# Kernel optimization log

Measured on AMD Instinct MI355X. Metric: run time of the kernel, lower is better.

The kernel has to match this reference:

```python
import jax, jax.numpy as jnp
import numpy as np
import math

S, B, H, NH = 2048, 2, 2048, 16
HN = H // NH  # head dim = 128

def setup_inputs() -> dict:
    key = jax.random.key(0)
    ks = jax.random.split(key, 5)
    hidden_states = jax.random.normal(ks[0], (S, B, H), dtype=jnp.float32)
    # causal mask: True means masked (filled with -10000), broadcast over heads
    attention_mask = jnp.triu(jnp.ones((S, S), dtype=bool), k=1)[None, None].repeat(B, axis=0)
    w_qkv = jax.random.normal(ks[1], (3 * H, H), dtype=jnp.float32) * (1.0 / math.sqrt(H))
    b_qkv = jax.random.normal(ks[2], (3 * H,), dtype=jnp.float32) * 0.02
    w_dense = jax.random.normal(ks[3], (H, H), dtype=jnp.float32) * (1.0 / math.sqrt(H))
    b_dense = jax.random.normal(ks[4], (H,), dtype=jnp.float32) * 0.02
    return {"hidden_states": hidden_states, "attention_mask": attention_mask,
            "w_qkv": w_qkv, "b_qkv": b_qkv, "w_dense": w_dense, "b_dense": b_dense}

def reference(hidden_states, attention_mask, w_qkv, b_qkv, w_dense, b_dense):
    s, b, h = hidden_states.shape
    nh, hn = NH, h // NH
    # QKV projection (ColumnParallelLinear, world_size=1)
    qkv = hidden_states @ w_qkv.T + b_qkv                # [s, b, 3h]
    qkv = qkv.reshape(s, b, nh, 3 * hn)
    q, k, v = jnp.split(qkv, 3, axis=-1)                 # each [s, b, nh, hn]
    q = q.transpose(1, 2, 0, 3)                          # [b, nh, s, hn]
    k = k.transpose(1, 2, 0, 3)
    v = v.transpose(1, 2, 0, 3)
    # norm_factor = sqrt(hn)*coeff, softmax rescales by coeff -> net 1/sqrt(hn)
    scores = jnp.einsum('bnqh,bnkh->bnqk', q, k) / jnp.float32(math.sqrt(hn))
    scores = jnp.where(attention_mask, jnp.float32(-10000.0), scores)
    probs = jax.nn.softmax(scores, axis=-1)              # [b, nh, s, s]
    ctx = jnp.einsum('bnqk,bnkh->bnqh', probs, v)        # [b, nh, s, hn]
    ctx = ctx.transpose(2, 0, 1, 3).reshape(s, b, h)     # [s, b, h]
    # RowParallelLinear with skip_bias_add=True: bias returned separately
    output = ctx @ w_dense.T
    return output, b_dense
```

## Files before the change

kernel.cpp:

```cpp
#include <hip/hip_runtime.h>

typedef unsigned short u16;
typedef unsigned int   u32;
typedef __attribute__((ext_vector_type(8))) short bf16x8;
typedef __attribute__((ext_vector_type(4))) float f32x4;

#define S_LEN 2048
#define B_SZ  2
#define H_DIM 2048
#define NH_   16
#define HN_   128
#define M_TOK 4096
#define NQKV  6144
#define NT_   (S_LEN / 64)

#define LGKM_BARRIER asm volatile("s_waitcnt lgkmcnt(0)\n\ts_barrier" ::: "memory")
#define SCHED_FENCE  asm volatile("" ::: "memory")

__device__ __forceinline__ u16 f2bf(float f) {
    u32 x = __float_as_uint(f);
    return (u16)((x + 0x7fffu + ((x >> 16) & 1u)) >> 16);
}

__device__ __forceinline__ void async16(const void* g, void* l) {
    __builtin_amdgcn_global_load_lds((const __attribute__((address_space(1))) void*)g,
                                     (__attribute__((address_space(3))) void*)l,
                                     16, 0, 0);
}

__global__ __launch_bounds__(256) void cvt3(
    const float* __restrict__ a, u16* __restrict__ oa, int na,
    const float* __restrict__ b, u16* __restrict__ ob, int nb,
    const float* __restrict__ c, u16* __restrict__ oc, int nc)
{
    int g = blockIdx.x * 256 + threadIdx.x;
    const float* in; u16* out; int idx;
    if (g < na)           { in = a; out = oa; idx = g; }
    else if (g < na + nb) { in = b; out = ob; idx = g - na; }
    else if (g < na + nb + nc) { in = c; out = oc; idx = g - na - nb; }
    else return;
    int i = idx * 4;
    float4 v = *(const float4*)&in[i];
    ushort4 o;
    o.x = f2bf(v.x); o.y = f2bf(v.y); o.z = f2bf(v.z); o.w = f2bf(v.w);
    *(ushort4*)&out[i] = o;
}

template<int EPI>
__global__ __launch_bounds__(256) void gemm_rs(
    const u16* __restrict__ A, const u16* __restrict__ W,
    const float* __restrict__ bias, float* __restrict__ Cout,
    u16* __restrict__ Qb, u16* __restrict__ Kb, u16* __restrict__ Vt,
    int M, int N, int K)
{
    __shared__ __align__(16) u16 Af[2][8 * 64 * 8];
    __shared__ __align__(16) u16 Bf[2][8 * 64 * 8];
    const int t = threadIdx.x, l = t & 63, w = t >> 6;
    const int quad = l >> 4, ln = l & 15;
    const int wm = w >> 1, wn = w & 1;
    const int m0 = blockIdx.y * 128, n0 = blockIdx.x * 128;

    const int c0 = t, c1 = t + 256;
    const u16* pa0 = &A[(size_t)(m0 + (c0 >> 6) * 16 + (c0 & 15)) * K + ((c0 >> 4) & 3) * 8];
    const u16* pa1 = &A[(size_t)(m0 + (c1 >> 6) * 16 + (c1 & 15)) * K + ((c1 >> 4) & 3) * 8];
    const u16* pb0 = &W[(size_t)(n0 + (c0 >> 6) * 16 + (c0 & 15)) * K + ((c0 >> 4) & 3) * 8];
    const u16* pb1 = &W[(size_t)(n0 + (c1 >> 6) * 16 + (c1 & 15)) * K + ((c1 >> 4) & 3) * 8];

    f32x4 acc[4][4];
#pragma unroll
    for (int i = 0; i < 4; ++i)
#pragma unroll
        for (int j = 0; j < 4; ++j)
#pragma unroll
            for (int r = 0; r < 4; ++r) acc[i][j][r] = 0.f;

    bf16x8 xa0, xa1, xb0, xb1;
    bf16x8 ya0, ya1, yb0, yb1;

#define LD_TILE(k0, a0, a1, b0, b1)                 \
    do {                                            \
        a0 = *(const bf16x8*)(pa0 + (k0));          \
        a1 = *(const bf16x8*)(pa1 + (k0));          \
        b0 = *(const bf16x8*)(pb0 + (k0));          \
        b1 = *(const bf16x8*)(pb1 + (k0));          \
        SCHED_FENCE;                                \
    } while (0)

#define ST_TILE(buf, a0, a1, b0, b1)                \
    do {                                            \
        *(bf16x8*)&Af[buf][t * 8]        = a0;      \
        *(bf16x8*)&Af[buf][t * 8 + 2048] = a1;      \
        *(bf16x8*)&Bf[buf][t * 8]        = b0;      \
        *(bf16x8*)&Bf[buf][t * 8 + 2048] = b1;      \
    } while (0)

#define COMPUTE(buf)                                                          \
    do {                                                                      \
        bf16x8 af[4], bfr[4];                                                 \
        _Pragma("unroll")                                                     \
        for (int x = 0; x < 4; ++x) {                                         \
            af[x]  = *(const bf16x8*)&Af[buf][((wm * 4 + x) * 64 + l) * 8];   \
            bfr[x] = *(const bf16x8*)&Bf[buf][((wn * 4 + x) * 64 + l) * 8];   \
        }                                                                     \
        _Pragma("unroll")                                                     \
        for (int mt = 0; mt < 4; ++mt)                                        \
            _Pragma("unroll")                                                 \
            for (int nt = 0; nt < 4; ++nt)                                    \
                acc[mt][nt] = __builtin_amdgcn_mfma_f32_16x16x32_bf16(        \
                    af[mt], bfr[nt], acc[mt][nt], 0, 0, 0);                   \
    } while (0)

    const int NIT = K / 32;

    LD_TILE(0, xa0, xa1, xb0, xb1);
    ST_TILE(0, xa0, xa1, xb0, xb1);
    LD_TILE(32, ya0, ya1, yb0, yb1);
    LGKM_BARRIER;

#pragma unroll 1
    for (int kk = 0; kk < NIT; kk += 2) {
        if (kk + 2 < NIT) LD_TILE((kk + 2) * 32, xa0, xa1, xb0, xb1);
        COMPUTE(0);
        ST_TILE(1, ya0, ya1, yb0, yb1);
        LGKM_BARRIER;
        if (kk + 3 < NIT) LD_TILE((kk + 3) * 32, ya0, ya1, yb0, yb1);
        COMPUTE(1);
        if (kk + 2 < NIT) ST_TILE(0, xa0, xa1, xb0, xb1);
        LGKM_BARRIER;
    }
#undef LD_TILE
#undef ST_TILE
#undef COMPUTE

    if constexpr (EPI == 0) {
#pragma unroll
        for (int mt = 0; mt < 4; ++mt)
#pragma unroll
            for (int nt = 0; nt < 4; ++nt) {
                int col = n0 + (wn * 4 + nt) * 16 + ln;
#pragma unroll
                for (int r = 0; r < 4; ++r) {
                    int row = m0 + wm * 64 + mt * 16 + quad * 4 + r;
                    Cout[(size_t)row * N + col] = acc[mt][nt][r];
                }
            }
    } else {
        const float kQS = 0.08838834764831845f * 1.44269504088896340f;
#pragma unroll
        for (int nt = 0; nt < 4; ++nt) {
            int col  = n0 + (wn * 4 + nt) * 16 + ln;
            int head = col / 384;
            int g    = col - head * 384;
            int sec  = g >> 7;
            int d    = g & 127;
            float bv = bias[col];
#pragma unroll
            for (int mt = 0; mt < 4; ++mt)
#pragma unroll
                for (int r = 0; r < 4; ++r) {
                    int tok = m0 + wm * 64 + mt * 16 + quad * 4 + r;
                    int s = tok >> 1, bb = tok & 1;
                    float v = acc[mt][nt][r] + bv;
                    if (sec == 0)
                        Qb[((size_t)(bb * NH_ + head) * S_LEN + s) * HN_ + d] = f2bf(v * kQS);
                    else if (sec == 1)
                        Kb[((size_t)(bb * NH_ + head) * S_LEN + s) * HN_ + d] = f2bf(v);
                    else
                        Vt[((size_t)(bb * NH_ + head) * HN_ + d) * S_LEN + s] = f2bf(v);
                }
        }
    }
}

__global__ __launch_bounds__(256) void attn_mfma(
    const u16* __restrict__ Qb, const u16* __restrict__ Kb,
    const u16* __restrict__ Vt, u16* __restrict__ Ctx)
{
    __shared__ __align__(16) u16 Ks[2][16 * 64 * 8];
    __shared__ __align__(16) u16 Vs[2][16 * 64 * 8];
    __shared__ __align__(16) u16 Psm[4][16][72];

    const int t = threadIdx.x, l = t & 63, w = t >> 6;
    const int quad = l >> 4, ln = l & 15;
    const int j = blockIdx.x;
    const int n = blockIdx.y, b = blockIdx.z;
    const u16* Qh = Qb + (size_t)(b * NH_ + n) * S_LEN * HN_;
    const u16* Kh = Kb + (size_t)(b * NH_ + n) * S_LEN * HN_;
    const u16* Vh = Vt + (size_t)(b * NH_ + n) * HN_ * S_LEN;

#pragma unroll 1
    for (int phase = 0; phase < 2; ++phase) {
        const int qt = phase ? j : (NT_ - 1 - j);
        const int q0 = qt * 64;

#pragma unroll
        for (int i = 0; i < 4; ++i)
            async16(&Qh[(size_t)(q0 + i * 16 + ln) * HN_ + w * 32 + quad * 8],
                    &Ks[1][((i * 4 + w) * 64 + l) * 8]);
#pragma unroll
        for (int i = 0; i < 4; ++i) {
            async16(&Kh[(size_t)(i * 16 + ln) * HN_ + w * 32 + quad * 8],
                    &Ks[0][((i * 4 + w) * 64 + l) * 8]);
            int dv = i * 4 + w, dt = dv >> 1, ks = dv & 1;
            async16(&Vh[(size_t)(dt * 16 + ln) * S_LEN + ks * 32 + quad * 8],
                    &Vs[0][(dv * 64 + l) * 8]);
        }
        __syncthreads();

        bf16x8 qf[4];
#pragma unroll
        for (int ks = 0; ks < 4; ++ks)
            qf[ks] = *(const bf16x8*)&Ks[1][((w * 4 + ks) * 64 + l) * 8];
        __syncthreads();

        float m_i[4], l_i[4];
        f32x4 acco[8];
#pragma unroll
        for (int r = 0; r < 4; ++r) { m_i[r] = -1e30f; l_i[r] = 0.f; }
#pragma unroll
        for (int dt = 0; dt < 8; ++dt)
#pragma unroll
            for (int r = 0; r < 4; ++r) acco[dt][r] = 0.f;

#pragma unroll 1
        for (int kt = 0; kt <= qt; ++kt) {
            const int cur = kt & 1;

            if (kt < qt) {
                const int nxt = cur ^ 1;
#pragma unroll
                for (int i = 0; i < 4; ++i) {
                    async16(&Kh[(size_t)((kt + 1) * 64 + i * 16 + ln) * HN_ + w * 32 + quad * 8],
                            &Ks[nxt][((i * 4 + w) * 64 + l) * 8]);
                    int dv = i * 4 + w, dt = dv >> 1, ks = dv & 1;
                    async16(&Vh[(size_t)(dt * 16 + ln) * S_LEN + (kt + 1) * 64 + ks * 32 + quad * 8],
                            &Vs[nxt][(dv * 64 + l) * 8]);
                }
            }

            f32x4 sc[4];
#pragma unroll
            for (int nt = 0; nt < 4; ++nt)
#pragma unroll
                for (int r = 0; r < 4; ++r) sc[nt][r] = 0.f;
#pragma unroll
            for (int nt = 0; nt < 4; ++nt)
#pragma unroll
                for (int ks = 0; ks < 4; ++ks) {
                    bf16x8 kf = *(const bf16x8*)&Ks[cur][((nt * 4 + ks) * 64 + l) * 8];
                    sc[nt] = __builtin_amdgcn_mfma_f32_16x16x32_bf16(qf[ks], kf, sc[nt], 0, 0, 0);
                }

            if (kt == qt) {
#pragma unroll
                for (int nt = 0; nt < 4; ++nt)
#pragma unroll
                    for (int r = 0; r < 4; ++r)
                        if (nt * 16 + ln > w * 16 + quad * 4 + r) sc[nt][r] = -1e30f;
            }

            float corr[4];
#pragma unroll
            for (int r = 0; r < 4; ++r) {
                float mx = fmaxf(fmaxf(sc[0][r], sc[1][r]), fmaxf(sc[2][r], sc[3][r]));
                mx = fmaxf(mx, __shfl_xor(mx, 1));
                mx = fmaxf(mx, __shfl_xor(mx, 2));
                mx = fmaxf(mx, __shfl_xor(mx, 4));
                mx = fmaxf(mx, __shfl_xor(mx, 8));
                float mnew = fmaxf(m_i[r], mx);
                corr[r] = exp2f(m_i[r] - mnew);
                m_i[r] = mnew;
            }
#pragma unroll
            for (int r = 0; r < 4; ++r) {
                float ps = 0.f;
#pragma unroll
                for (int nt = 0; nt < 4; ++nt) {
                    float p = exp2f(sc[nt][r] - m_i[r]);
                    ps += p;
                    Psm[w][quad * 4 + r][nt * 16 + ln] = f2bf(p);
                }
                l_i[r] = l_i[r] * corr[r] + ps;
            }

#pragma unroll
            for (int dt = 0; dt < 8; ++dt)
#pragma unroll
                for (int r = 0; r < 4; ++r) acco[dt][r] *= corr[r];

            bf16x8 pf[2];
#pragma unroll
            for (int ks = 0; ks < 2; ++ks)
                pf[ks] = *(const bf16x8*)&Psm[w][ln][ks * 32 + quad * 8];
#pragma unroll
            for (int dt = 0; dt < 8; ++dt)
#pragma unroll
                for (int ks = 0; ks < 2; ++ks) {
                    bf16x8 vf = *(const bf16x8*)&Vs[cur][((dt * 2 + ks) * 64 + l) * 8];
                    acco[dt] = __builtin_amdgcn_mfma_f32_16x16x32_bf16(pf[ks], vf, acco[dt], 0, 0, 0);
                }
            __syncthreads();
        }

#pragma unroll
        for (int r = 0; r < 4; ++r) {
            float s = l_i[r];
            s += __shfl_xor(s, 1);
            s += __shfl_xor(s, 2);
            s += __shfl_xor(s, 4);
            s += __shfl_xor(s, 8);
            l_i[r] = 1.f / s;
        }
#pragma unroll
        for (int dt = 0; dt < 8; ++dt)
#pragma unroll
            for (int r = 0; r < 4; ++r) {
                int srow = q0 + w * 16 + quad * 4 + r;
                Ctx[((size_t)(srow * B_SZ + b)) * H_DIM + n * HN_ + dt * 16 + ln] =
                    f2bf(acco[dt][r] * l_i[r]);
            }
    }
}

__global__ void copy_bias(const float* __restrict__ b_dense, float* __restrict__ out)
{
    int t = blockIdx.x * 256 + threadIdx.x;
    if (t < H_DIM) out[(size_t)M_TOK * H_DIM + t] = b_dense[t];
}

extern "C" void kernel_launch(void* const* d_in, const int* in_sizes, int n_in,
                              void* d_out, int out_size, void* d_ws, size_t ws_size,
                              hipStream_t stream)
{
    const float* hs      = (const float*)d_in[0];
    const float* w_qkv   = (const float*)d_in[2];
    const float* b_qkv   = (const float*)d_in[3];
    const float* w_dense = (const float*)d_in[4];
    const float* b_dense = (const float*)d_in[5];
    float* out = (float*)d_out;

    u16* hs_bf = (u16*)d_ws;
    u16* wq_bf = hs_bf + (size_t)M_TOK * H_DIM;
    u16* wd_bf = wq_bf + (size_t)NQKV * H_DIM;
    u16* Qb    = wd_bf + (size_t)H_DIM * H_DIM;
    u16* Kb    = Qb    + (size_t)M_TOK * H_DIM;
    u16* Vt    = Kb    + (size_t)M_TOK * H_DIM;
    u16* Ctx   = Vt    + (size_t)M_TOK * H_DIM;

    const int g1 = (M_TOK * H_DIM) / 4;
    const int g2 = (NQKV * H_DIM) / 4;
    const int g3 = (H_DIM * H_DIM) / 4;
    cvt3<<<(g1 + g2 + g3 + 255) / 256, 256, 0, stream>>>(
        hs, hs_bf, g1, w_qkv, wq_bf, g2, w_dense, wd_bf, g3);

    gemm_rs<1><<<dim3(NQKV / 128, M_TOK / 128), 256, 0, stream>>>(
        hs_bf, wq_bf, b_qkv, nullptr, Qb, Kb, Vt, M_TOK, NQKV, H_DIM);

    attn_mfma<<<dim3(NT_ / 2, NH_, B_SZ), 256, 0, stream>>>(Qb, Kb, Vt, Ctx);

    gemm_rs<0><<<dim3(H_DIM / 128, M_TOK / 128), 256, 0, stream>>>(
        Ctx, wd_bf, nullptr, out, nullptr, nullptr, nullptr, M_TOK, H_DIM, H_DIM);

    copy_bias<<<(H_DIM + 255) / 256, 256, 0, stream>>>(b_dense, out);
}
```

Measured before the change: 502.6 us.

## Replace GEMM with 256x256 tiled 8-wave kernel using async LDS loads and swizzle

Both projection GEMMs now use a new kernel with 256x256 output tiles, 512 threads, and 64-wide K steps. Tiles go straight from global memory into XOR-swizzled shared memory through async loads, interleaved with MFMA quarter-blocks under raised wave priority. Workgroups are remapped so that neighbouring blocks land across XCDs. The aim is more data reuse per tile, fewer LDS bank conflicts, and latency hidden behind compute. The cost is heavier register and shared-memory use, many barriers, and sizes hardcoded at compile time.

New measurement: 450.4 us. 1.12x faster.

```diff
diff --git a/kernel.cpp b/kernel.cpp
--- a/kernel.cpp
+++ b/kernel.cpp
@@ -14,8 +14,8 @@
 #define NQKV  6144
 #define NT_   (S_LEN / 64)
 
-#define LGKM_BARRIER asm volatile("s_waitcnt lgkmcnt(0)\n\ts_barrier" ::: "memory")
-#define SCHED_FENCE  asm volatile("" ::: "memory")
+#define BAR      asm volatile("s_barrier" ::: "memory")
+#define WAITV(n) asm volatile("s_waitcnt vmcnt(" #n ")" ::: "memory")
 
 __device__ __forceinline__ u16 f2bf(float f) {
     u32 x = __float_as_uint(f);
@@ -46,128 +46,185 @@
     *(ushort4*)&out[i] = o;
 }
 
-template<int EPI>
-__global__ __launch_bounds__(256) void gemm_rs(
+template<int EPI, int MM, int NN>
+__global__ __launch_bounds__(512, 2) void gemm8(
     const u16* __restrict__ A, const u16* __restrict__ W,
     const float* __restrict__ bias, float* __restrict__ Cout,
-    u16* __restrict__ Qb, u16* __restrict__ Kb, u16* __restrict__ Vt,
-    int M, int N, int K)
+    u16* __restrict__ Qb, u16* __restrict__ Kb, u16* __restrict__ Vt)
 {
-    __shared__ __align__(16) u16 Af[2][8 * 64 * 8];
-    __shared__ __align__(16) u16 Bf[2][8 * 64 * 8];
+    constexpr int K   = 2048;
+    constexpr int NKT = K / 64;
+    constexpr int NBN = NN / 256;
+    constexpr int NWG = (MM / 256) * NBN;
+
+    __shared__ __align__(16) u16 sA[2][256 * 64];
+    __shared__ __align__(16) u16 sB[2][256 * 64];
+
     const int t = threadIdx.x, l = t & 63, w = t >> 6;
     const int quad = l >> 4, ln = l & 15;
-    const int wm = w >> 1, wn = w & 1;
-    const int m0 = blockIdx.y * 128, n0 = blockIdx.x * 128;
-
-    const int c0 = t, c1 = t + 256;
-    const u16* pa0 = &A[(size_t)(m0 + (c0 >> 6) * 16 + (c0 & 15)) * K + ((c0 >> 4) & 3) * 8];
-    const u16* pa1 = &A[(size_t)(m0 + (c1 >> 6) * 16 + (c1 & 15)) * K + ((c1 >> 4) & 3) * 8];
-    const u16* pb0 = &W[(size_t)(n0 + (c0 >> 6) * 16 + (c0 & 15)) * K + ((c0 >> 4) & 3) * 8];
-    const u16* pb1 = &W[(size_t)(n0 + (c1 >> 6) * 16 + (c1 & 15)) * K + ((c1 >> 4) & 3) * 8];
-
-    f32x4 acc[4][4];
-#pragma unroll
-    for (int i = 0; i < 4; ++i)
-#pragma unroll
-        for (int j = 0; j < 4; ++j)
-#pragma unroll
-            for (int r = 0; r < 4; ++r) acc[i][j][r] = 0.f;
-
-    bf16x8 xa0, xa1, xb0, xb1;
-    bf16x8 ya0, ya1, yb0, yb1;
-
-#define LD_TILE(k0, a0, a1, b0, b1)                 \
-    do {                                            \
-        a0 = *(const bf16x8*)(pa0 + (k0));          \
-        a1 = *(const bf16x8*)(pa1 + (k0));          \
-        b0 = *(const bf16x8*)(pb0 + (k0));          \
-        b1 = *(const bf16x8*)(pb1 + (k0));          \
-        SCHED_FENCE;                                \
+    const int qw_r = w >> 2, qw_c = w & 3;
+
+    int wg = blockIdx.x;
+    wg = (wg & 7) * (NWG / 8) + (wg >> 3);
+    const int m0 = (wg / NBN) * 256, n0 = (wg % NBN) * 256;
+
+    const int srow = t >> 3;
+    const int skc  = (t & 7) ^ (srow & 7);
+    const u16* pA = A + (size_t)(m0 + srow) * K + skc * 8;
+    const u16* pB = W + (size_t)(n0 + srow) * K + skc * 8;
+
+#define STAGE_A(db, h, kt)                                                        \
+    do {                                                                          \
+        async16(pA + (size_t)(h) * 128 * K + (size_t)(kt) * 64,                   \
+                &sA[db][(h) * 8192 + t * 8]);                                     \
+        async16(pA + (size_t)(h) * 128 * K + (size_t)64 * K + (size_t)(kt) * 64,  \
+                &sA[db][(h) * 8192 + t * 8 + 4096]);                              \
     } while (0)
-
-#define ST_TILE(buf, a0, a1, b0, b1)                \
-    do {                                            \
-        *(bf16x8*)&Af[buf][t * 8]        = a0;      \
-        *(bf16x8*)&Af[buf][t * 8 + 2048] = a1;      \
-        *(bf16x8*)&Bf[buf][t * 8]        = b0;      \
-        *(bf16x8*)&Bf[buf][t * 8 + 2048] = b1;      \
+#define STAGE_B(db, h, kt)                                                        \
+    do {                                                                          \
+        async16(pB + (size_t)(h) * 128 * K + (size_t)(kt) * 64,                   \
+                &sB[db][(h) * 8192 + t * 8]);                                     \
+        async16(pB + (size_t)(h) * 128 * K + (size_t)64 * K + (size_t)(kt) * 64,  \
+                &sB[db][(h) * 8192 + t * 8 + 4096]);                              \
     } while (0)
 
-#define COMPUTE(buf)                                                          \
-    do {                                                                      \
-        bf16x8 af[4], bfr[4];                                                 \
-        _Pragma("unroll")                                                     \
-        for (int x = 0; x < 4; ++x) {                                         \
-            af[x]  = *(const bf16x8*)&Af[buf][((wm * 4 + x) * 64 + l) * 8];   \
-            bfr[x] = *(const bf16x8*)&Bf[buf][((wn * 4 + x) * 64 + l) * 8];   \
-        }                                                                     \
-        _Pragma("unroll")                                                     \
-        for (int mt = 0; mt < 4; ++mt)                                        \
-            _Pragma("unroll")                                                 \
-            for (int nt = 0; nt < 4; ++nt)                                    \
-                acc[mt][nt] = __builtin_amdgcn_mfma_f32_16x16x32_bf16(        \
-                    af[mt], bfr[nt], acc[mt][nt], 0, 0, 0);                   \
+    const int aBase = (qw_r * 64 + ln) * 64;
+    const int bBase = (qw_c * 32 + ln) * 64;
+    int swz[2];
+#pragma unroll
+    for (int ks = 0; ks < 2; ++ks)
+        swz[ks] = ((ks * 4 + quad) ^ (ln & 7)) << 3;
+
+    bf16x8 af[4][2];
+    bf16x8 bf[2][2];
+
+#define RD_A(db, mq)                                                              \
+    do {                                                                          \
+        _Pragma("unroll") for (int mf = 0; mf < 4; ++mf)                          \
+        _Pragma("unroll") for (int ks = 0; ks < 2; ++ks)                          \
+            af[mf][ks] = *(const bf16x8*)&sA[db][aBase + (mq) * 8192 + mf * 1024  \
+                                                + swz[ks]];                       \
     } while (0)
-
-    const int NIT = K / 32;
-
-    LD_TILE(0, xa0, xa1, xb0, xb1);
-    ST_TILE(0, xa0, xa1, xb0, xb1);
-    LD_TILE(32, ya0, ya1, yb0, yb1);
-    LGKM_BARRIER;
+#define RD_B(db, nq)                                                              \
+    do {                                                                          \
+        _Pragma("unroll") for (int nf = 0; nf < 2; ++nf)                          \
+        _Pragma("unroll") for (int ks = 0; ks < 2; ++ks)                          \
+            bf[nf][ks] = *(const bf16x8*)&sB[db][bBase + (nq) * 8192 + nf * 1024  \
+                                                + swz[ks]];                       \
+    } while (0)
+
+    f32x4 acc[4][4][2];
+#pragma unroll
+    for (int q = 0; q < 4; ++q)
+#pragma unroll
+        for (int mf = 0; mf < 4; ++mf)
+#pragma unroll
+            for (int nf = 0; nf < 2; ++nf)
+#pragma unroll
+                for (int r = 0; r < 4; ++r) acc[q][mf][nf][r] = 0.f;
+
+#define MM16(q)                                                                   \
+    do {                                                                          \
+        __builtin_amdgcn_s_setprio(1);                                            \
+        _Pragma("unroll") for (int mf = 0; mf < 4; ++mf)                          \
+        _Pragma("unroll") for (int nf = 0; nf < 2; ++nf)                          \
+        _Pragma("unroll") for (int ks = 0; ks < 2; ++ks)                          \
+            acc[q][mf][nf] = __builtin_amdgcn_mfma_f32_16x16x32_bf16(             \
+                af[mf][ks], bf[nf][ks], acc[q][mf][nf], 0, 0, 0);                 \
+        __builtin_amdgcn_s_setprio(0);                                            \
+    } while (0)
+
+    STAGE_A(0, 0, 0); STAGE_B(0, 0, 0); STAGE_A(0, 1, 0); STAGE_B(0, 1, 0);
+    STAGE_A(1, 0, 1); STAGE_B(1, 0, 1);
+    WAITV(4);
+    BAR;
 
 #pragma unroll 1
-    for (int kk = 0; kk < NIT; kk += 2) {
-        if (kk + 2 < NIT) LD_TILE((kk + 2) * 32, xa0, xa1, xb0, xb1);
-        COMPUTE(0);
-        ST_TILE(1, ya0, ya1, yb0, yb1);
-        LGKM_BARRIER;
-        if (kk + 3 < NIT) LD_TILE((kk + 3) * 32, ya0, ya1, yb0, yb1);
-        COMPUTE(1);
-        if (kk + 2 < NIT) ST_TILE(0, xa0, xa1, xb0, xb1);
-        LGKM_BARRIER;
+    for (int i = 0; i < NKT / 2; ++i) {
+        const int tt  = 2 * i;
+        const int tp1 = tt + 1;
+        const int tp2 = (tt + 2) & (NKT - 1);
+        const int tp3 = (tt + 3) & (NKT - 1);
+
+        RD_A(0, 0); RD_B(0, 0);
+        STAGE_A(1, 1, tp1);
+        BAR; MM16(0); BAR;
+        RD_B(0, 1);
+        STAGE_B(1, 1, tp1);
+        BAR; MM16(1); BAR;
+        RD_A(0, 1); RD_B(0, 0);
+        STAGE_A(0, 0, tp2);
+        BAR; MM16(2); BAR;
+        RD_B(0, 1);
+        STAGE_B(0, 0, tp2);
+        BAR; MM16(3);
+        WAITV(4);
+        BAR;
+        RD_A(1, 0); RD_B(1, 0);
+        STAGE_A(0, 1, tp2);
+        BAR; MM16(0); BAR;
+        RD_B(1, 1);
+        STAGE_B(0, 1, tp2);
+        BAR; MM16(1); BAR;
+        RD_A(1, 1); RD_B(1, 0);
+        STAGE_A(1, 0, tp3);
+        BAR; MM16(2); BAR;
+        RD_B(1, 1);
+        STAGE_B(1, 0, tp3);
+        BAR; MM16(3);
+        WAITV(4);
+        BAR;
     }
-#undef LD_TILE
-#undef ST_TILE
-#undef COMPUTE
+#undef STAGE_A
+#undef STAGE_B
+#undef RD_A
+#undef RD_B
+#undef MM16
 
     if constexpr (EPI == 0) {
 #pragma unroll
-        for (int mt = 0; mt < 4; ++mt)
-#pragma unroll
-            for (int nt = 0; nt < 4; ++nt) {
-                int col = n0 + (wn * 4 + nt) * 16 + ln;
-#pragma unroll
-                for (int r = 0; r < 4; ++r) {
-                    int row = m0 + wm * 64 + mt * 16 + quad * 4 + r;
-                    Cout[(size_t)row * N + col] = acc[mt][nt][r];
+        for (int q = 0; q < 4; ++q) {
+            const int mq = q >> 1, nq = q & 1;
+#pragma unroll
+            for (int mf = 0; mf < 4; ++mf)
+#pragma unroll
+                for (int nf = 0; nf < 2; ++nf) {
+                    int col = n0 + nq * 128 + qw_c * 32 + nf * 16 + ln;
+#pragma unroll
+                    for (int r = 0; r < 4; ++r) {
+                        int row = m0 + mq * 128 + qw_r * 64 + mf * 16 + quad * 4 + r;
+                        Cout[(size_t)row * NN + col] = acc[q][mf][nf][r];
+                    }
                 }
-            }
+        }
     } else {
         const float kQS = 0.08838834764831845f * 1.44269504088896340f;
 #pragma unroll
-        for (int nt = 0; nt < 4; ++nt) {
-            int col  = n0 + (wn * 4 + nt) * 16 + ln;
-            int head = col / 384;
-            int g    = col - head * 384;
-            int sec  = g >> 7;
-            int d    = g & 127;
-            float bv = bias[col];
-#pragma unroll
-            for (int mt = 0; mt < 4; ++mt)
-#pragma unroll
-                for (int r = 0; r < 4; ++r) {
-                    int tok = m0 + wm * 64 + mt * 16 + quad * 4 + r;
-                    int s = tok >> 1, bb = tok & 1;
-                    float v = acc[mt][nt][r] + bv;
-                    if (sec == 0)
-                        Qb[((size_t)(bb * NH_ + head) * S_LEN + s) * HN_ + d] = f2bf(v * kQS);
-                    else if (sec == 1)
-                        Kb[((size_t)(bb * NH_ + head) * S_LEN + s) * HN_ + d] = f2bf(v);
-                    else
-                        Vt[((size_t)(bb * NH_ + head) * HN_ + d) * S_LEN + s] = f2bf(v);
-                }
+        for (int q = 0; q < 4; ++q) {
+            const int mq = q >> 1, nq = q & 1;
+#pragma unroll
+            for (int nf = 0; nf < 2; ++nf) {
+                int col  = n0 + nq * 128 + qw_c * 32 + nf * 16 + ln;
+                int head = col / 384;
+                int g    = col - head * 384;
+                int sec  = g >> 7;
+                int d    = g & 127;
+                float bv = bias[col];
+#pragma unroll
+                for (int mf = 0; mf < 4; ++mf)
+#pragma unroll
+                    for (int r = 0; r < 4; ++r) {
+                        int tok = m0 + mq * 128 + qw_r * 64 + mf * 16 + quad * 4 + r;
+                        int s = tok >> 1, bb = tok & 1;
+                        float v = acc[q][mf][nf][r] + bv;
+                        if (sec == 0)
+                            Qb[((size_t)(bb * NH_ + head) * S_LEN + s) * HN_ + d] = f2bf(v * kQS);
+                        else if (sec == 1)
+                            Kb[((size_t)(bb * NH_ + head) * S_LEN + s) * HN_ + d] = f2bf(v);
+                        else
+                            Vt[((size_t)(bb * NH_ + head) * HN_ + d) * S_LEN + s] = f2bf(v);
+                    }
+            }
         }
     }
 }
@@ -353,13 +410,13 @@
     cvt3<<<(g1 + g2 + g3 + 255) / 256, 256, 0, stream>>>(
         hs, hs_bf, g1, w_qkv, wq_bf, g2, w_dense, wd_bf, g3);
 
-    gemm_rs<1><<<dim3(NQKV / 128, M_TOK / 128), 256, 0, stream>>>(
-        hs_bf, wq_bf, b_qkv, nullptr, Qb, Kb, Vt, M_TOK, NQKV, H_DIM);
+    gemm8<1, M_TOK, NQKV><<<(M_TOK / 256) * (NQKV / 256), 512, 0, stream>>>(
+        hs_bf, wq_bf, b_qkv, nullptr, Qb, Kb, Vt);
 
     attn_mfma<<<dim3(NT_ / 2, NH_, B_SZ), 256, 0, stream>>>(Qb, Kb, Vt, Ctx);
 
-    gemm_rs<0><<<dim3(H_DIM / 128, M_TOK / 128), 256, 0, stream>>>(
-        Ctx, wd_bf, nullptr, out, nullptr, nullptr, nullptr, M_TOK, H_DIM, H_DIM);
+    gemm8<0, M_TOK, H_DIM><<<(M_TOK / 256) * (H_DIM / 256), 512, 0, stream>>>(
+        Ctx, wd_bf, nullptr, out, nullptr, nullptr, nullptr);
 
     copy_bias<<<(H_DIM + 255) / 256, 256, 0, stream>>>(b_dense, out);
 }
```
